# Kernel optimization log

Measured on AMD Instinct MI355X. Metric: run time of the kernel, lower is better.

Reference implementation:

```python
import jax, jax.numpy as jnp
import numpy as np

B, T, D_IN, D_OUT = 4, 2048, 1024, 1024

def setup_inputs() -> dict:
    key = jax.random.key(0)
    k0, k1, k2, k3 = jax.random.split(key, 4)
    s = 1.0 / np.sqrt(D_IN)
    return {
        "x": jax.random.normal(k0, (B, T, D_IN), dtype=jnp.float32),
        "w_query": jax.random.normal(k1, (D_OUT, D_IN), dtype=jnp.float32) * s,
        "w_key": jax.random.normal(k2, (D_OUT, D_IN), dtype=jnp.float32) * s,
        "w_value": jax.random.normal(k3, (D_OUT, D_IN), dtype=jnp.float32) * s,
    }

def reference(x, w_query, w_key, w_value):
    # Linear (no bias): y = x @ W.T, W has shape (d_out, d_in)
    q = jnp.einsum('btd,od->bto', x, w_query)   # (B,T,d_out)
    k = jnp.einsum('btd,od->bto', x, w_key)
    v = jnp.einsum('btd,od->bto', x, w_value)
    scale = 1.0 / jnp.sqrt(jnp.asarray(k.shape[-1], dtype=x.dtype))
    scores = jnp.einsum('bqo,bko->bqk', q, k) * scale  # (B,T,T)
    t = scores.shape[-1]
    causal = jnp.tril(jnp.ones((t, t), dtype=bool))    # True = keep
    scores = jnp.where(causal, scores, -jnp.inf)
    weights = jax.nn.softmax(scores, axis=-1)
    # dropout rate is 0.0 -> identity
    context = jnp.einsum('bqk,bko->bqo', weights, v)   # (B,T,d_out)
    return context
```

## Files before the change

kernel.cpp:

```cpp
#include <hip/hip_runtime.h>
#include <hip/hip_bf16.h>

#define NB 4
#define TT 2048
#define DD 1024
#define MM (NB*TT)

using f32x4  = __attribute__((ext_vector_type(4))) float;
using bf16x8 = __attribute__((ext_vector_type(8))) __bf16;
using u16x8  = __attribute__((ext_vector_type(8))) unsigned short;

__device__ __forceinline__ unsigned short f2b(float f) {
  __hip_bfloat16 h = __float2bfloat16(f);
  return *reinterpret_cast<unsigned short*>(&h);
}

__device__ __forceinline__ float b2f(unsigned short u) {
  __hip_bfloat16 h = *reinterpret_cast<__hip_bfloat16*>(&u);
  return __bfloat162float(h);
}

__device__ __forceinline__ void gld_lds16(const void* g, void* l) {
  __builtin_amdgcn_global_load_lds(
      (const __attribute__((address_space(1))) void*)g,
      (__attribute__((address_space(3))) void*)l, 16, 0, 0);
}

__global__ void k_cvt4(const float* __restrict__ x,  const float* __restrict__ wq,
                       const float* __restrict__ wk, const float* __restrict__ wv,
                       unsigned short* __restrict__ xb, unsigned short* __restrict__ wqb,
                       unsigned short* __restrict__ wkb, unsigned short* __restrict__ wvb) {
  const int nx = MM*DD/4, nw = DD*DD/4;
  const int ntot = nx + 3*nw;
  int i = blockIdx.x * blockDim.x + threadIdx.x;
  int stride = gridDim.x * blockDim.x;
  for (; i < ntot; i += stride) {
    const float* s; unsigned short* d; int j;
    if (i < nx)            { s = x;  d = xb;  j = i; }
    else if (i < nx + nw)  { s = wq; d = wqb; j = i - nx; }
    else if (i < nx + 2*nw){ s = wk; d = wkb; j = i - nx - nw; }
    else                   { s = wv; d = wvb; j = i - nx - 2*nw; }
    float4 v = reinterpret_cast<const float4*>(s)[j];
    ushort4 o;
    o.x = f2b(v.x); o.y = f2b(v.y); o.z = f2b(v.z); o.w = f2b(v.w);
    reinterpret_cast<ushort4*>(d)[j] = o;
  }
}

__launch_bounds__(256)
__global__ void k_qkv(const unsigned short* __restrict__ xb,
                      const unsigned short* __restrict__ wqb,
                      const unsigned short* __restrict__ wkb,
                      const unsigned short* __restrict__ wvb,
                      unsigned short* __restrict__ Qb,
                      unsigned short* __restrict__ Kb,
                      unsigned short* __restrict__ Vt) {
  __shared__ __align__(16) unsigned short As[128*64];
  __shared__ __align__(16) unsigned short Bs[128*64];
  const int tid = threadIdx.x;
  const int l = tid & 63, wid = tid >> 6;
  const int z = blockIdx.z;
  const unsigned short* W = (z == 0) ? wqb : (z == 1) ? wkb : wvb;
  unsigned short* out = (z == 0) ? Qb : (z == 1) ? Kb : Vt;
  const long m0 = (long)blockIdx.x * 128;
  const long n0 = (long)blockIdx.y * 128;
  const int l15 = l & 15, l4 = l >> 4;
  const int wr = (wid >> 1) * 64, wc = (wid & 1) * 64;

  const int srow = wid * 8 + (l >> 3);
  const int scol = 8 * ((l & 7) ^ (l >> 3));
  const unsigned short* Ap = xb + (m0 + srow) * DD + scol;
  const unsigned short* Wp = W  + (n0 + srow) * DD + scol;
  unsigned short* AsW = &As[wid * 512];
  unsigned short* BsW = &Bs[wid * 512];

  f32x4 acc[4][4] = {};

  for (int k0 = 0; k0 < DD; k0 += 64) {
    __syncthreads();
    #pragma unroll
    for (int u = 0; u < 4; ++u) {
      gld_lds16(Ap + (size_t)u*32*DD + k0, AsW + u*2048);
      gld_lds16(Wp + (size_t)u*32*DD + k0, BsW + u*2048);
    }
    __syncthreads();
    #pragma unroll
    for (int kk = 0; kk < 2; ++kk) {
      bf16x8 af[4], bfr[4];
      #pragma unroll
      for (int mi = 0; mi < 4; ++mi) {
        int ro = wr + mi*16 + l15;
        int off = ro*128 + ((kk*64 + l4*16) ^ ((ro & 7) << 4));
        af[mi] = *reinterpret_cast<const bf16x8*>((const char*)As + off);
      }
      #pragma unroll
      for (int ni = 0; ni < 4; ++ni) {
        int ro = wc + ni*16 + l15;
        int off = ro*128 + ((kk*64 + l4*16) ^ ((ro & 7) << 4));
        bfr[ni] = *reinterpret_cast<const bf16x8*>((const char*)Bs + off);
      }
      #pragma unroll
      for (int mi = 0; mi < 4; ++mi)
        #pragma unroll
        for (int ni = 0; ni < 4; ++ni)
          acc[mi][ni] = __builtin_amdgcn_mfma_f32_16x16x32_bf16(af[mi], bfr[ni], acc[mi][ni], 0, 0, 0);
    }
  }

  if (z < 2) {
    #pragma unroll
    for (int mi = 0; mi < 4; ++mi)
      #pragma unroll
      for (int ni = 0; ni < 4; ++ni)
        #pragma unroll
        for (int r = 0; r < 4; ++r) {
          long row = m0 + wr + mi*16 + l4*4 + r;
          long col = n0 + wc + ni*16 + l15;
          out[row * DD + col] = f2b(acc[mi][ni][r]);
        }
  } else {
    #pragma unroll
    for (int mi = 0; mi < 4; ++mi)
      #pragma unroll
      for (int ni = 0; ni < 4; ++ni)
        #pragma unroll
        for (int r = 0; r < 4; ++r) {
          long row = m0 + wr + mi*16 + l4*4 + r;
          long col = n0 + wc + ni*16 + l15;
          long b = row >> 11, t = row & (TT - 1);
          out[(b * DD + col) * TT + t] = f2b(acc[mi][ni][r]);
        }
  }
}

__launch_bounds__(256)
__global__ void k_scores(const unsigned short* __restrict__ Qb,
                         const unsigned short* __restrict__ Kb,
                         unsigned short* __restrict__ S) {
  __shared__ __align__(16) unsigned short As[128*64];
  __shared__ __align__(16) unsigned short Bs[128*64];
  const int tid = threadIdx.x;
  const int l = tid & 63, wid = tid >> 6;
  const int l15 = l & 15, l4 = l >> 4;
  const int wr = (wid >> 1) * 64, wc = (wid & 1) * 64;

  const int bid = blockIdx.x;
  const int swz = (bid & 7) * 68 + (bid >> 3);
  const int b = swz / 136;
  int t = swz % 136;
  int qi = 0;
  while ((qi + 1) * (qi + 2) / 2 <= t) qi++;
  const int ki = t - qi * (qi + 1) / 2;

  const size_t arow0 = (size_t)b * TT + qi * 128;
  const size_t brow0 = (size_t)b * TT + ki * 128;

  const int srow = wid * 8 + (l >> 3);
  const int scol = 8 * ((l & 7) ^ (l >> 3));
  const unsigned short* Ap = Qb + (arow0 + srow) * DD + scol;
  const unsigned short* Bp = Kb + (brow0 + srow) * DD + scol;
  unsigned short* AsW = &As[wid * 512];
  unsigned short* BsW = &Bs[wid * 512];

  f32x4 acc[4][4] = {};

  for (int k0 = 0; k0 < DD; k0 += 64) {
    __syncthreads();
    #pragma unroll
    for (int u = 0; u < 4; ++u) {
      gld_lds16(Ap + (size_t)u*32*DD + k0, AsW + u*2048);
      gld_lds16(Bp + (size_t)u*32*DD + k0, BsW + u*2048);
    }
    __syncthreads();
    #pragma unroll
    for (int kk = 0; kk < 2; ++kk) {
      bf16x8 af[4], bfr[4];
      #pragma unroll
      for (int mi = 0; mi < 4; ++mi) {
        int ro = wr + mi*16 + l15;
        int off = ro*128 + ((kk*64 + l4*16) ^ ((ro & 7) << 4));
        af[mi] = *reinterpret_cast<const bf16x8*>((const char*)As + off);
      }
      #pragma unroll
      for (int ni = 0; ni < 4; ++ni) {
        int ro = wc + ni*16 + l15;
        int off = ro*128 + ((kk*64 + l4*16) ^ ((ro & 7) << 4));
        bfr[ni] = *reinterpret_cast<const bf16x8*>((const char*)Bs + off);
      }
      #pragma unroll
      for (int mi = 0; mi < 4; ++mi)
        #pragma unroll
        for (int ni = 0; ni < 4; ++ni)
          acc[mi][ni] = __builtin_amdgcn_mfma_f32_16x16x32_bf16(af[mi], bfr[ni], acc[mi][ni], 0, 0, 0);
    }
  }

  const float scale = 0.03125f;
  #pragma unroll
  for (int mi = 0; mi < 4; ++mi)
    #pragma unroll
    for (int ni = 0; ni < 4; ++ni)
      #pragma unroll
      for (int r = 0; r < 4; ++r) {
        int row = wr + mi*16 + l4*4 + r;
        int col = wc + ni*16 + l15;
        int gq = qi*128 + row, gk = ki*128 + col;
        float v = (gk > gq) ? -1e30f : acc[mi][ni][r] * scale;
        S[((size_t)b * TT + gq) * TT + gk] = f2b(v);
      }
}

__launch_bounds__(256)
__global__ void k_softmax(unsigned short* __restrict__ S, float* __restrict__ rl) {
  const int tid = threadIdx.x;
  const int w = tid >> 6, l = tid & 63;
  const int row = blockIdx.x * 4 + w;
  const int b = row >> 11, q = row & (TT - 1);
  unsigned short* Srow = S + ((size_t)b * TT + q) * TT;
  const int width = ((q >> 7) + 1) << 7;

  float v[4][8];
  bool has[4];
  float mx = -1e30f;
  #pragma unroll
  for (int c = 0; c < 4; ++c) {
    const int off = c * 512 + l * 8;
    has[c] = off < width;
    if (has[c]) {
      u16x8 u = *reinterpret_cast<const u16x8*>(&Srow[off]);
      #pragma unroll
      for (int j = 0; j < 8; ++j) { v[c][j] = b2f(u[j]); mx = fmaxf(mx, v[c][j]); }
    }
  }
  #pragma unroll
  for (int mm = 1; mm < 64; mm <<= 1) mx = fmaxf(mx, __shfl_xor(mx, mm));

  float s = 0.f;
  #pragma unroll
  for (int c = 0; c < 4; ++c) {
    if (has[c]) {
      u16x8 u;
      #pragma unroll
      for (int j = 0; j < 8; ++j) {
        float p = __expf(v[c][j] - mx);
        s += p;
        u[j] = f2b(p);
      }
      *reinterpret_cast<u16x8*>(&Srow[c * 512 + l * 8]) = u;
    }
  }
  #pragma unroll
  for (int mm = 1; mm < 64; mm <<= 1) s += __shfl_xor(s, mm);
  if (l == 0) rl[row] = 1.0f / s;
}

__launch_bounds__(256)
__global__ void k_pv(const unsigned short* __restrict__ P,
                     const unsigned short* __restrict__ Vt,
                     const float* __restrict__ rl,
                     float* __restrict__ O) {
  __shared__ __align__(16) unsigned short As[128*64];
  __shared__ __align__(16) unsigned short Bs[128*64];
  const int tid = threadIdx.x;
  const int l = tid & 63, wid = tid >> 6;
  const int l15 = l & 15, l4 = l >> 4;
  const int wr = (wid >> 1) * 64, wc = (wid & 1) * 64;

  const int qi = 15 - (blockIdx.x >> 5);
  const int di = (blockIdx.x >> 2) & 7;
  const int b  = blockIdx.x & 3;
  const int KEXT = (qi + 1) * 128;

  const int srow = wid * 8 + (l >> 3);
  const int scol = 8 * ((l & 7) ^ (l >> 3));
  const unsigned short* Ap = P  + ((size_t)b * TT + qi * 128 + srow) * TT + scol;
  const unsigned short* Bp = Vt + ((size_t)b * DD + di * 128 + srow) * TT + scol;
  unsigned short* AsW = &As[wid * 512];
  unsigned short* BsW = &Bs[wid * 512];

  f32x4 acc[4][4] = {};

  for (int k0 = 0; k0 < KEXT; k0 += 64) {
    __syncthreads();
    #pragma unroll
    for (int u = 0; u < 4; ++u) {
      gld_lds16(Ap + (size_t)u*32*TT + k0, AsW + u*2048);
      gld_lds16(Bp + (size_t)u*32*TT + k0, BsW + u*2048);
    }
    __syncthreads();
    #pragma unroll
    for (int kk = 0; kk < 2; ++kk) {
      bf16x8 af[4], bfr[4];
      #pragma unroll
      for (int mi = 0; mi < 4; ++mi) {
        int ro = wr + mi*16 + l15;
        int off = ro*128 + ((kk*64 + l4*16) ^ ((ro & 7) << 4));
        af[mi] = *reinterpret_cast<const bf16x8*>((const char*)As + off);
      }
      #pragma unroll
      for (int ni = 0; ni < 4; ++ni) {
        int ro = wc + ni*16 + l15;
        int off = ro*128 + ((kk*64 + l4*16) ^ ((ro & 7) << 4));
        bfr[ni] = *reinterpret_cast<const bf16x8*>((const char*)Bs + off);
      }
      #pragma unroll
      for (int mi = 0; mi < 4; ++mi)
        #pragma unroll
        for (int ni = 0; ni < 4; ++ni)
          acc[mi][ni] = __builtin_amdgcn_mfma_f32_16x16x32_bf16(af[mi], bfr[ni], acc[mi][ni], 0, 0, 0);
    }
  }

  #pragma unroll
  for (int mi = 0; mi < 4; ++mi)
    #pragma unroll
    for (int ni = 0; ni < 4; ++ni)
      #pragma unroll
      for (int r = 0; r < 4; ++r) {
        int row = wr + mi*16 + l4*4 + r;
        int col = wc + ni*16 + l15;
        size_t q = (size_t)qi * 128 + row;
        O[((size_t)b * TT + q) * DD + di * 128 + col] =
            acc[mi][ni][r] * rl[(size_t)b * TT + q];
      }
}

extern "C" void kernel_launch(void* const* d_in, const int* in_sizes, int n_in,
                              void* d_out, int out_size, void* d_ws, size_t ws_size,
                              hipStream_t stream) {
  const float* x  = (const float*)d_in[0];
  const float* wq = (const float*)d_in[1];
  const float* wk = (const float*)d_in[2];
  const float* wv = (const float*)d_in[3];
  unsigned short* ws  = (unsigned short*)d_ws;
  unsigned short* Qb  = ws;
  unsigned short* Kb  = Qb + (size_t)MM * DD;
  unsigned short* Vt  = Kb + (size_t)MM * DD;
  unsigned short* Sb  = Vt + (size_t)MM * DD;
  unsigned short* xb  = Sb;
  unsigned short* wqb = xb + (size_t)MM * DD;
  unsigned short* wkb = wqb + (size_t)DD * DD;
  unsigned short* wvb = wkb + (size_t)DD * DD;
  float* rl = (float*)(Sb + (size_t)NB * TT * TT);
  float* out = (float*)d_out;

  k_cvt4<<<2048, 256, 0, stream>>>(x, wq, wk, wv, xb, wqb, wkb, wvb);
  k_qkv<<<dim3(MM/128, DD/128, 3), 256, 0, stream>>>(xb, wqb, wkb, wvb, Qb, Kb, Vt);
  k_scores<<<544, 256, 0, stream>>>(Qb, Kb, Sb);
  k_softmax<<<MM/4, 256, 0, stream>>>(Sb, rl);
  k_pv<<<512, 256, 0, stream>>>(Sb, Vt, rl, out);
}
```

Baseline: 158.6 us.

## Fold Wq and Wk into one Gram matrix to skip K projection

Rewrites scores as x·(Wq^T Wk)·x^T. A 1024x1024 matrix G is precomputed from transposed bf16 weights, and Y = x·G replaces the separate Q and K projections, so one of the three large projection GEMMs disappears. The scores kernel then multiplies Y by x directly. This adds a small transpose kernel and a DxD GEMM, and rounding G and Y to bf16 changes numerical error compared with computing Q and K separately.

```diff
diff --git a/kernel.cpp b/kernel.cpp
--- a/kernel.cpp
+++ b/kernel.cpp
@@ -26,20 +26,16 @@
       (__attribute__((address_space(3))) void*)l, 16, 0, 0);
 }
 
-__global__ void k_cvt4(const float* __restrict__ x,  const float* __restrict__ wq,
-                       const float* __restrict__ wk, const float* __restrict__ wv,
-                       unsigned short* __restrict__ xb, unsigned short* __restrict__ wqb,
-                       unsigned short* __restrict__ wkb, unsigned short* __restrict__ wvb) {
+__global__ void k_cvt2(const float* __restrict__ x, const float* __restrict__ wv,
+                       unsigned short* __restrict__ xb, unsigned short* __restrict__ wvb) {
   const int nx = MM*DD/4, nw = DD*DD/4;
-  const int ntot = nx + 3*nw;
+  const int ntot = nx + nw;
   int i = blockIdx.x * blockDim.x + threadIdx.x;
   int stride = gridDim.x * blockDim.x;
   for (; i < ntot; i += stride) {
     const float* s; unsigned short* d; int j;
-    if (i < nx)            { s = x;  d = xb;  j = i; }
-    else if (i < nx + nw)  { s = wq; d = wqb; j = i - nx; }
-    else if (i < nx + 2*nw){ s = wk; d = wkb; j = i - nx - nw; }
-    else                   { s = wv; d = wvb; j = i - nx - 2*nw; }
+    if (i < nx) { s = x;  d = xb;  j = i; }
+    else        { s = wv; d = wvb; j = i - nx; }
     float4 v = reinterpret_cast<const float4*>(s)[j];
     ushort4 o;
     o.x = f2b(v.x); o.y = f2b(v.y); o.z = f2b(v.z); o.w = f2b(v.w);
@@ -48,20 +44,109 @@
 }
 
 __launch_bounds__(256)
-__global__ void k_qkv(const unsigned short* __restrict__ xb,
-                      const unsigned short* __restrict__ wqb,
-                      const unsigned short* __restrict__ wkb,
-                      const unsigned short* __restrict__ wvb,
-                      unsigned short* __restrict__ Qb,
-                      unsigned short* __restrict__ Kb,
-                      unsigned short* __restrict__ Vt) {
+__global__ void k_cvtT(const float* __restrict__ wq, const float* __restrict__ wk,
+                       unsigned short* __restrict__ wqT, unsigned short* __restrict__ wkT) {
+  __shared__ unsigned short tile[64][72];
+  const float* src = blockIdx.z ? wk : wq;
+  unsigned short* dst = blockIdx.z ? wkT : wqT;
+  const int o0 = blockIdx.x * 64, d0 = blockIdx.y * 64;
+  const int tid = threadIdx.x;
+  const int r = tid >> 2;
+  const int c = (tid & 3) * 16;
+  #pragma unroll
+  for (int j = 0; j < 16; j += 4) {
+    float4 v = *reinterpret_cast<const float4*>(&src[(size_t)(o0 + r) * DD + d0 + c + j]);
+    tile[c + j + 0][r] = f2b(v.x);
+    tile[c + j + 1][r] = f2b(v.y);
+    tile[c + j + 2][r] = f2b(v.z);
+    tile[c + j + 3][r] = f2b(v.w);
+  }
+  __syncthreads();
+  #pragma unroll
+  for (int j = 0; j < 16; j += 8) {
+    u16x8 u;
+    #pragma unroll
+    for (int jj = 0; jj < 8; ++jj) u[jj] = tile[r][c + j + jj];
+    *reinterpret_cast<u16x8*>(&dst[(size_t)(d0 + r) * DD + o0 + c + j]) = u;
+  }
+}
+
+__launch_bounds__(256)
+__global__ void k_g(const unsigned short* __restrict__ wkT,
+                    const unsigned short* __restrict__ wqT,
+                    unsigned short* __restrict__ Gt) {
+  __shared__ __align__(16) unsigned short As[64*64];
+  __shared__ __align__(16) unsigned short Bs[64*64];
+  const int tid = threadIdx.x;
+  const int l = tid & 63, wid = tid >> 6;
+  const int l15 = l & 15, l4 = l >> 4;
+  const int wr = (wid >> 1) * 32, wc = (wid & 1) * 32;
+  const int m0 = blockIdx.x * 64, n0 = blockIdx.y * 64;
+
+  const int srow = wid * 8 + (l >> 3);
+  const int scol = 8 * ((l & 7) ^ (l >> 3));
+  const unsigned short* Ap = wkT + (size_t)(m0 + srow) * DD + scol;
+  const unsigned short* Bp = wqT + (size_t)(n0 + srow) * DD + scol;
+  unsigned short* AsW = &As[wid * 512];
+  unsigned short* BsW = &Bs[wid * 512];
+
+  f32x4 acc[2][2] = {};
+
+  for (int k0 = 0; k0 < DD; k0 += 64) {
+    __syncthreads();
+    #pragma unroll
+    for (int u = 0; u < 2; ++u) {
+      gld_lds16(Ap + (size_t)u*32*DD + k0, AsW + u*2048);
+      gld_lds16(Bp + (size_t)u*32*DD + k0, BsW + u*2048);
+    }
+    __syncthreads();
+    #pragma unroll
+    for (int kk = 0; kk < 2; ++kk) {
+      bf16x8 af[2], bfr[2];
+      #pragma unroll
+      for (int mi = 0; mi < 2; ++mi) {
+        int ro = wr + mi*16 + l15;
+        int off = ro*128 + ((kk*64 + l4*16) ^ ((ro & 7) << 4));
+        af[mi] = *reinterpret_cast<const bf16x8*>((const char*)As + off);
+      }
+      #pragma unroll
+      for (int ni = 0; ni < 2; ++ni) {
+        int ro = wc + ni*16 + l15;
+        int off = ro*128 + ((kk*64 + l4*16) ^ ((ro & 7) << 4));
+        bfr[ni] = *reinterpret_cast<const bf16x8*>((const char*)Bs + off);
+      }
+      #pragma unroll
+      for (int mi = 0; mi < 2; ++mi)
+        #pragma unroll
+        for (int ni = 0; ni < 2; ++ni)
+          acc[mi][ni] = __builtin_amdgcn_mfma_f32_16x16x32_bf16(af[mi], bfr[ni], acc[mi][ni], 0, 0, 0);
+    }
+  }
+
+  #pragma unroll
+  for (int mi = 0; mi < 2; ++mi)
+    #pragma unroll
+    for (int ni = 0; ni < 2; ++ni)
+      #pragma unroll
+      for (int r = 0; r < 4; ++r) {
+        int row = wr + mi*16 + l4*4 + r;
+        int col = wc + ni*16 + l15;
+        Gt[(size_t)(m0 + row) * DD + n0 + col] = f2b(acc[mi][ni][r]);
+      }
+}
+
+__launch_bounds__(256)
+__global__ void k_yv(const unsigned short* __restrict__ xb,
+                     const unsigned short* __restrict__ Gtb,
+                     const unsigned short* __restrict__ wvb,
+                     unsigned short* __restrict__ Y,
+                     unsigned short* __restrict__ Vt) {
   __shared__ __align__(16) unsigned short As[128*64];
   __shared__ __align__(16) unsigned short Bs[128*64];
   const int tid = threadIdx.x;
   const int l = tid & 63, wid = tid >> 6;
   const int z = blockIdx.z;
-  const unsigned short* W = (z == 0) ? wqb : (z == 1) ? wkb : wvb;
-  unsigned short* out = (z == 0) ? Qb : (z == 1) ? Kb : Vt;
+  const unsigned short* W = z ? wvb : Gtb;
   const long m0 = (long)blockIdx.x * 128;
   const long n0 = (long)blockIdx.y * 128;
   const int l15 = l & 15, l4 = l >> 4;
@@ -107,7 +192,7 @@
     }
   }
 
-  if (z < 2) {
+  if (z == 0) {
     #pragma unroll
     for (int mi = 0; mi < 4; ++mi)
       #pragma unroll
@@ -116,7 +201,7 @@
         for (int r = 0; r < 4; ++r) {
           long row = m0 + wr + mi*16 + l4*4 + r;
           long col = n0 + wc + ni*16 + l15;
-          out[row * DD + col] = f2b(acc[mi][ni][r]);
+          Y[row * DD + col] = f2b(acc[mi][ni][r]);
         }
   } else {
     #pragma unroll
@@ -128,14 +213,14 @@
           long row = m0 + wr + mi*16 + l4*4 + r;
           long col = n0 + wc + ni*16 + l15;
           long b = row >> 11, t = row & (TT - 1);
-          out[(b * DD + col) * TT + t] = f2b(acc[mi][ni][r]);
+          Vt[(b * DD + col) * TT + t] = f2b(acc[mi][ni][r]);
         }
   }
 }
 
 __launch_bounds__(256)
-__global__ void k_scores(const unsigned short* __restrict__ Qb,
-                         const unsigned short* __restrict__ Kb,
+__global__ void k_scores(const unsigned short* __restrict__ Yb,
+                         const unsigned short* __restrict__ xb,
                          unsigned short* __restrict__ S) {
   __shared__ __align__(16) unsigned short As[128*64];
   __shared__ __align__(16) unsigned short Bs[128*64];
@@ -157,8 +242,8 @@
 
   const int srow = wid * 8 + (l >> 3);
   const int scol = 8 * ((l & 7) ^ (l >> 3));
-  const unsigned short* Ap = Qb + (arow0 + srow) * DD + scol;
-  const unsigned short* Bp = Kb + (brow0 + srow) * DD + scol;
+  const unsigned short* Ap = Yb + (arow0 + srow) * DD + scol;
+  const unsigned short* Bp = xb + (brow0 + srow) * DD + scol;
   unsigned short* AsW = &As[wid * 512];
   unsigned short* BsW = &Bs[wid * 512];
 
@@ -333,20 +418,22 @@
   const float* wk = (const float*)d_in[2];
   const float* wv = (const float*)d_in[3];
   unsigned short* ws  = (unsigned short*)d_ws;
-  unsigned short* Qb  = ws;
-  unsigned short* Kb  = Qb + (size_t)MM * DD;
-  unsigned short* Vt  = Kb + (size_t)MM * DD;
+  unsigned short* xb  = ws;
+  unsigned short* Y   = xb + (size_t)MM * DD;
+  unsigned short* Vt  = Y  + (size_t)MM * DD;
   unsigned short* Sb  = Vt + (size_t)MM * DD;
-  unsigned short* xb  = Sb;
-  unsigned short* wqb = xb + (size_t)MM * DD;
-  unsigned short* wkb = wqb + (size_t)DD * DD;
-  unsigned short* wvb = wkb + (size_t)DD * DD;
+  unsigned short* wvb = Sb;
+  unsigned short* wqT = wvb + (size_t)DD * DD;
+  unsigned short* wkT = wqT + (size_t)DD * DD;
+  unsigned short* Gt  = wkT + (size_t)DD * DD;
   float* rl = (float*)(Sb + (size_t)NB * TT * TT);
   float* out = (float*)d_out;
 
-  k_cvt4<<<2048, 256, 0, stream>>>(x, wq, wk, wv, xb, wqb, wkb, wvb);
-  k_qkv<<<dim3(MM/128, DD/128, 3), 256, 0, stream>>>(xb, wqb, wkb, wvb, Qb, Kb, Vt);
-  k_scores<<<544, 256, 0, stream>>>(Qb, Kb, Sb);
+  k_cvt2<<<2048, 256, 0, stream>>>(x, wv, xb, wvb);
+  k_cvtT<<<dim3(16, 16, 2), 256, 0, stream>>>(wq, wk, wqT, wkT);
+  k_g<<<dim3(16, 16), 256, 0, stream>>>(wkT, wqT, Gt);
+  k_yv<<<dim3(MM/128, DD/128, 2), 256, 0, stream>>>(xb, Gt, wvb, Y, Vt);
+  k_scores<<<544, 256, 0, stream>>>(Y, xb, Sb);
   k_softmax<<<MM/4, 256, 0, stream>>>(Sb, rl);
   k_pv<<<512, 256, 0, stream>>>(Sb, Vt, rl, out);
 }
```

New measurement: 153.1 us, median of 2. -3.5%, faster.
